# Performance work log

Hardware: AMD Instinct MI355X
Metric: run time of the kernel (lower is better)

The kernel has to match this reference:

```python
import jax, jax.numpy as jnp
import numpy as np

N_ORDER = 256
PRED_LEN = 192
SEQ_LEN = 768
ENC_IN = 21
BATCH = 16
MULTISCALE = [1, 2, 4]
MODES = 32  # min(32, min(pred_len, seq_len)//2)


def _transition(N):
    Q = np.arange(N, dtype=np.float64)
    R = (2 * Q + 1)[:, None]
    j, i = np.meshgrid(Q, Q)
    A = np.where(i < j, -1, (-1.0) ** (i - j + 1)) * R
    B = (-1.0) ** Q[:, None] * R
    return A, B


def _bilinear(A, B, dt):
    # scipy cont2discrete(method='bilinear'): Ad=(I-dt/2 A)^-1 (I+dt/2 A), Bd=(I-dt/2 A)^-1 dt B
    N = A.shape[0]
    I = np.eye(N)
    ima = I - (dt / 2.0) * A
    Ad = np.linalg.solve(ima, I + (dt / 2.0) * A)
    Bd = np.linalg.solve(ima, dt * B)
    return Ad, Bd.squeeze(-1)


def _legendre_eval(N, x):
    # Legendre P_n(x) via three-term recurrence; returns [len(x), N]
    T = x.shape[0]
    P = np.zeros((N, T))
    P[0] = 1.0
    if N > 1:
        P[1] = x
    for n in range(2, N):
        P[n] = ((2 * n - 1) * x * P[n - 1] - (n - 1) * P[n - 2]) / n
    return P.T


def setup_inputs() -> dict:
    key = jax.random.key(0)
    ks = jax.random.split(key, 12)
    inp = {"x_enc": jax.random.normal(ks[0], (BATCH, SEQ_LEN, ENC_IN), dtype=jnp.float32)}
    Ac, Bc = _transition(N_ORDER)
    scale = 1.0 / (N_ORDER * N_ORDER)
    for idx, m in enumerate(MULTISCALE):
        dt = 1.0 / PRED_LEN / m
        Ad, Bd = _bilinear(Ac, Bc, dt)
        vals = np.arange(0.0, 1.0, dt)
        E = _legendre_eval(N_ORDER, 1.0 - 2.0 * vals)
        inp[f"A{idx}"] = jnp.asarray(Ad, jnp.float32)
        inp[f"B{idx}"] = jnp.asarray(Bd, jnp.float32)
        inp[f"E{idx}"] = jnp.asarray(E, jnp.float32)
        inp[f"Wr{idx}"] = scale * jax.random.uniform(ks[1 + 2 * idx], (N_ORDER, N_ORDER, MODES), dtype=jnp.float32)
        inp[f"Wi{idx}"] = scale * jax.random.uniform(ks[2 + 2 * idx], (N_ORDER, N_ORDER, MODES), dtype=jnp.float32)
    inp["mlp_w"] = 0.1 * jax.random.normal(ks[10], (1, len(MULTISCALE)), dtype=jnp.float32)
    inp["mlp_b"] = jnp.zeros((1,), jnp.float32)
    return inp


def _hippo(x, A, Bv):
    # x: [B, E, L]; c_t = c_{t-1} @ A^T + f_t * B  (F.linear(c, A) == c @ A.T)
    def step(c, f):
        c = c @ A.T + f[..., None] * Bv
        return c, c
    c0 = jnp.zeros(x.shape[:-1] + (A.shape[0],), x.dtype)
    _, cs = jax.lax.scan(step, c0, jnp.moveaxis(x, -1, 0))
    return jnp.moveaxis(cs, 0, -1)  # [B, E, N, L]


def _spec_conv(x, Wr, Wi):
    # x: [B, E, N_in, L]; keep first MODES rfft modes, complex channel mix, irfft
    L = x.shape[-1]
    a = jnp.fft.rfft(x, axis=-1)[..., :MODES]
    W = (Wr + 1j * Wi).astype(jnp.complex64)
    out = jnp.einsum('bjix,iox->bjox', a, W)
    nf = L // 2 + 1
    out_full = jnp.pad(out, ((0, 0), (0, 0), (0, 0), (0, nf - MODES)))
    return jnp.fft.irfft(out_full, n=L, axis=-1)


def reference(x_enc, A0, B0, E0, Wr0, Wi0, A1, B1, E1, Wr1, Wi1, A2, B2, E2, Wr2, Wi2, mlp_w, mlp_b):
    params = [(A0, B0, E0, Wr0, Wi0), (A1, B1, E1, Wr1, Wi1), (A2, B2, E2, Wr2, Wi2)]
    x_decs = []
    for m, (A, Bv, E, Wr, Wi) in zip(MULTISCALE, params):
        x_in = x_enc[:, -m * PRED_LEN:]                      # [B, L, E]
        c = _hippo(jnp.transpose(x_in, (0, 2, 1)), A, Bv)    # [B, E, N, L]
        out1 = _spec_conv(c, Wr, Wi)                         # [B, E, N, L]
        x_dec_c = out1[:, :, :, PRED_LEN - 1]                # seq_len >= pred_len, jump_dist=0
        x_decs.append(x_dec_c @ E[-PRED_LEN:].T)             # [B, E, pred_len]
    x_dec = jnp.stack(x_decs, axis=-1)                       # [B, E, pred_len, 3]
    out = x_dec @ mlp_w[0] + mlp_b[0]                        # Linear(3,1) then squeeze
    return jnp.transpose(out, (0, 2, 1))                     # [B, pred_len, E]
```

## Files before the change

### kernel.cpp

```cpp
#include <hip/hip_runtime.h>
#include <math.h>

#define PI_F 3.14159265358979323846f

#define W_OFF    0
#define AP_OFF   344064
#define KT_OFF   737280
#define KTOT_OFF 995328
#define Y_OFF    1142784
#define S_OFF    1142784
#define F_OFF    1732608
#define QT_OFF   10579968
#define WS_FLOATS 27095040

__device__ __forceinline__ int off_w_f(int s)  { return 49152  * ((1 << s) - 1); }
__device__ __forceinline__ int qoff_f(int s)   { return 2359296 * ((1 << s) - 1); }
__device__ __forceinline__ int ktoff_f(int s)  { return 36864  * ((1 << s) - 1); }
__device__ __forceinline__ int foff_f(int s)   { return 1179648 * ((1 << s) - 1); }

template<bool BT>
__device__ __forceinline__ void gemm_tile(const float* __restrict__ A,
                                          const float* __restrict__ B,
                                          float* __restrict__ C,
                                          int M, int N, int ldc, int m0, int n0)
{
    __shared__ float As[16][68];
    __shared__ float Bs[16][68];
    const int tid = threadIdx.x;
    const int tx = tid & 15;
    const int ty = tid >> 4;
    const int r  = tid >> 2;
    const int kq = (tid & 3) << 2;

    float acc[4][4] = {{0.f,0.f,0.f,0.f},{0.f,0.f,0.f,0.f},
                       {0.f,0.f,0.f,0.f},{0.f,0.f,0.f,0.f}};

    for (int kk = 0; kk < 256; kk += 16) {
        float4 av = make_float4(0.f, 0.f, 0.f, 0.f);
        if (m0 + r < M)
            av = *(const float4*)(A + (size_t)(m0 + r) * 256 + kk + kq);
        As[kq + 0][r] = av.x; As[kq + 1][r] = av.y;
        As[kq + 2][r] = av.z; As[kq + 3][r] = av.w;

        if (BT) {
            float4 bv = make_float4(0.f, 0.f, 0.f, 0.f);
            if (n0 + r < N)
                bv = *(const float4*)(B + (size_t)(n0 + r) * 256 + kk + kq);
            Bs[kq + 0][r] = bv.x; Bs[kq + 1][r] = bv.y;
            Bs[kq + 2][r] = bv.z; Bs[kq + 3][r] = bv.w;
        } else {
            const int kb = tid >> 4;
            const int j4 = (tid & 15) << 2;
            float4 bv = *(const float4*)(B + (size_t)(kk + kb) * 256 + n0 + j4);
            *(float4*)(&Bs[kb][j4]) = bv;
        }
        __syncthreads();

        #pragma unroll
        for (int k = 0; k < 16; ++k) {
            float4 a4 = *(const float4*)(&As[k][ty << 2]);
            float4 b4 = *(const float4*)(&Bs[k][tx << 2]);
            acc[0][0] = fmaf(a4.x, b4.x, acc[0][0]);
            acc[0][1] = fmaf(a4.x, b4.y, acc[0][1]);
            acc[0][2] = fmaf(a4.x, b4.z, acc[0][2]);
            acc[0][3] = fmaf(a4.x, b4.w, acc[0][3]);
            acc[1][0] = fmaf(a4.y, b4.x, acc[1][0]);
            acc[1][1] = fmaf(a4.y, b4.y, acc[1][1]);
            acc[1][2] = fmaf(a4.y, b4.z, acc[1][2]);
            acc[1][3] = fmaf(a4.y, b4.w, acc[1][3]);
            acc[2][0] = fmaf(a4.z, b4.x, acc[2][0]);
            acc[2][1] = fmaf(a4.z, b4.y, acc[2][1]);
            acc[2][2] = fmaf(a4.z, b4.z, acc[2][2]);
            acc[2][3] = fmaf(a4.z, b4.w, acc[2][3]);
            acc[3][0] = fmaf(a4.w, b4.x, acc[3][0]);
            acc[3][1] = fmaf(a4.w, b4.y, acc[3][1]);
            acc[3][2] = fmaf(a4.w, b4.z, acc[3][2]);
            acc[3][3] = fmaf(a4.w, b4.w, acc[3][3]);
        }
        __syncthreads();
    }

    #pragma unroll
    for (int u = 0; u < 4; ++u) {
        int row = m0 + (ty << 2) + u;
        if (row < M) {
            float4 cv = make_float4(acc[u][0], acc[u][1], acc[u][2], acc[u][3]);
            *(float4*)(C + (size_t)row * ldc + n0 + (tx << 2)) = cv;
        }
    }
}

__device__ __forceinline__ void gemm_64x256(const float* __restrict__ A,
                                            const float* __restrict__ B,
                                            float* __restrict__ C, int ldc)
{
    __shared__ float As[16][68];
    __shared__ float Bs[16][260];

    const int tid = threadIdx.x;
    const int tx = tid & 15;
    const int ty = tid >> 4;
    const int ra  = tid >> 2;
    const int kqa = (tid & 3) << 2;

    float acc[4][4][4];
    #pragma unroll
    for (int j = 0; j < 4; ++j)
        #pragma unroll
        for (int u = 0; u < 4; ++u)
            #pragma unroll
            for (int v = 0; v < 4; ++v) acc[j][u][v] = 0.f;

    for (int kk = 0; kk < 256; kk += 16) {
        float4 av = *(const float4*)(A + (size_t)ra * 256 + kk + kqa);
        As[kqa + 0][ra] = av.x; As[kqa + 1][ra] = av.y;
        As[kqa + 2][ra] = av.z; As[kqa + 3][ra] = av.w;

        const float* bp = B + (size_t)tid * 256 + kk;
        float4 b0 = *(const float4*)(bp);
        float4 b1 = *(const float4*)(bp + 4);
        float4 b2 = *(const float4*)(bp + 8);
        float4 b3 = *(const float4*)(bp + 12);
        Bs[ 0][tid] = b0.x; Bs[ 1][tid] = b0.y; Bs[ 2][tid] = b0.z; Bs[ 3][tid] = b0.w;
        Bs[ 4][tid] = b1.x; Bs[ 5][tid] = b1.y; Bs[ 6][tid] = b1.z; Bs[ 7][tid] = b1.w;
        Bs[ 8][tid] = b2.x; Bs[ 9][tid] = b2.y; Bs[10][tid] = b2.z; Bs[11][tid] = b2.w;
        Bs[12][tid] = b3.x; Bs[13][tid] = b3.y; Bs[14][tid] = b3.z; Bs[15][tid] = b3.w;
        __syncthreads();

        #pragma unroll
        for (int kq = 0; kq < 16; ++kq) {
            float4 a  = *(const float4*)(&As[kq][4 * ty]);
            float4 c0 = *(const float4*)(&Bs[kq][4 * tx]);
            float4 c1 = *(const float4*)(&Bs[kq][4 * tx + 64]);
            float4 c2 = *(const float4*)(&Bs[kq][4 * tx + 128]);
            float4 c3 = *(const float4*)(&Bs[kq][4 * tx + 192]);
            float af[4]  = {a.x, a.y, a.z, a.w};
            float bf[16] = {c0.x, c0.y, c0.z, c0.w, c1.x, c1.y, c1.z, c1.w,
                            c2.x, c2.y, c2.z, c2.w, c3.x, c3.y, c3.z, c3.w};
            #pragma unroll
            for (int j = 0; j < 4; ++j)
                #pragma unroll
                for (int u = 0; u < 4; ++u)
                    #pragma unroll
                    for (int v = 0; v < 4; ++v)
                        acc[j][u][v] = fmaf(af[u], bf[j * 4 + v], acc[j][u][v]);
        }
        __syncthreads();
    }

    #pragma unroll
    for (int u = 0; u < 4; ++u) {
        int row = 4 * ty + u;
        #pragma unroll
        for (int j = 0; j < 4; ++j) {
            float4 cv = make_float4(acc[j][u][0], acc[j][u][1],
                                    acc[j][u][2], acc[j][u][3]);
            *(float4*)(C + (size_t)row * ldc + 4 * tx + 64 * j) = cv;
        }
    }
}

__global__ void k_init(const float* B0, const float* B1, const float* B2, float* ws)
{
    int s = blockIdx.x;
    const float* Bv = (s == 0) ? B0 : (s == 1) ? B1 : B2;
    ws[W_OFF + off_w_f(s) + threadIdx.x] = Bv[threadIdx.x];
}

__global__ void k_level(int n, const float* A0, const float* A1, const float* A2,
                        float* ws)
{
    int s = blockIdx.z;
    int L = 192 << s;
    const float* Ain = (s == 0) ? A0 : (s == 1) ? A1 : A2;
    float* wbase = ws + W_OFF + off_w_f(s);
    float* bufA  = ws + AP_OFF + s * 131072;
    float* bufB  = bufA + 65536;
    const float* src = (n == 0) ? Ain : (((n - 1) & 1) ? bufB : bufA);

    int y = blockIdx.y;
    if (y < 4) {
        int p2 = 1 << n;
        if (p2 >= L) return;
        int cnt = min(p2, L - p2);
        int m0 = y * 64;
        if (m0 >= cnt) return;
        gemm_tile<true>(wbase, src, wbase + (size_t)p2 * 256,
                        cnt, 256, 256, m0, blockIdx.x * 64);
    } else {
        if ((2 << n) >= L) return;
        float* dst = (n & 1) ? bufB : bufA;
        gemm_tile<false>(src, src, dst, 256, 256, 256, (y - 4) * 64, blockIdx.x * 64);
    }
}

__global__ void k_transpose(const float* Wr0, const float* Wi0,
                            const float* Wr1, const float* Wi1,
                            const float* Wr2, const float* Wi2, float* ws)
{
    int bid = blockIdx.x;
    int i  = bid & 255;
    int ri = (bid >> 8) & 1;
    int s  = bid >> 9;
    const float* W;
    if (s == 0)      W = ri ? Wi0 : Wr0;
    else if (s == 1) W = ri ? Wi1 : Wr1;
    else             W = ri ? Wi2 : Wr2;

    int o = threadIdx.x;
    int sri = s * 2 + ri;
    const float* Wrow = W + (size_t)i * 8192 + (size_t)o * 32;
    #pragma unroll
    for (int k = 0; k < 32; ++k) {
        ws[QT_OFF + ((size_t)(sri * 32 + k) * 256 + i) * 256 + o] = Wrow[k];
    }
}

__global__ void __launch_bounds__(256, 2)
k_gemm_Y3(const float* E0, const float* E1, const float* E2, float* __restrict__ ws)
{
    const int zz = blockIdx.x;
    const int s  = blockIdx.z;
    const int L  = 192 << s;
    const int z  = s * 64 + zz;
    const int m0 = blockIdx.y * 64;
    const float* E = (s == 0) ? E0 : (s == 1) ? E1 : E2;

    const float* Ap = E + (size_t)(L - 192) * 256 + (size_t)m0 * 256;
    const float* Bp = ws + QT_OFF + (size_t)z * 65536;
    float* Cp = ws + Y_OFF + (size_t)z * 49152 + (size_t)m0 * 256;
    gemm_64x256(Ap, Bp, Cp, 256);
}

__global__ void __launch_bounds__(256, 2)
k_gemm_Q3(float* __restrict__ ws)
{
    const int s = blockIdx.z;
    const int L = 192 << s;
    const int m0 = blockIdx.y * 64;
    if (m0 >= L) return;
    const int n0 = blockIdx.x * 256;

    const float* Ap = ws + W_OFF + off_w_f(s) + (size_t)m0 * 256;
    const float* Bp = ws + Y_OFF + (size_t)s * 3145728 + (size_t)n0 * 256;
    float* Cp = ws + QT_OFF + qoff_f(s) + (size_t)m0 * 12288 + n0;
    gemm_64x256(Ap, Bp, Cp, 12288);
}

__global__ void k_scanA(float* __restrict__ ws)
{
    const int c = blockIdx.x;
    const int k = blockIdx.y;
    const int s = blockIdx.z;
    const int L = 192 << s;
    const int C = L >> 4;
    const int p = threadIdx.x;

    __shared__ float twc[768], tws[768];
    for (int m = p; m < L; m += 192) {
        float ang = -2.f * PI_F * (float)m / (float)L;
        float ss, cc; sincosf(ang, &ss, &cc);
        twc[m] = cc; tws[m] = ss;
    }
    __syncthreads();

    const float* Qr = ws + QT_OFF + qoff_f(s) + (size_t)k * 192;
    const float* Qi = Qr + 6144;

    float ar = 0.f, ai = 0.f;
    const int d0 = c * C;
    int ph = (k * d0) % L;
    for (int j = 0; j < C; ++j) {
        int d = d0 + j;
        float qr = Qr[(size_t)d * 12288 + p];
        float qi = Qi[(size_t)d * 12288 + p];
        float cc = twc[ph], sn = tws[ph];
        ar = fmaf(cc, qr, fmaf(-sn, qi, ar));
        ai = fmaf(cc, qi, fmaf( sn, qr, ai));
        ph += k; if (ph >= L) ph -= L;
    }
    size_t sb = (size_t)((s * 32 + k) * 16 + c) * 384;
    ws[S_OFF + sb + p]       = ar;
    ws[S_OFF + sb + 192 + p] = ai;
}

__global__ void k_scanB(float* __restrict__ ws)
{
    const int c = blockIdx.x;
    const int k = blockIdx.y;
    const int s = blockIdx.z;
    const int L = 192 << s;
    const int C = L >> 4;
    const int p = threadIdx.x;

    __shared__ float twc[768], tws[768];
    for (int m = p; m < L; m += 192) {
        float ang = -2.f * PI_F * (float)m / (float)L;
        float ss, cc; sincosf(ang, &ss, &cc);
        twc[m] = cc; tws[m] = ss;
    }
    __syncthreads();

    float ar = 0.f, ai = 0.f;
    size_t sbase = (size_t)(s * 32 + k) * 16 * 384;
    for (int c2 = 0; c2 < c; ++c2) {
        ar += ws[S_OFF + sbase + (size_t)c2 * 384 + p];
        ai += ws[S_OFF + sbase + (size_t)c2 * 384 + 192 + p];
    }

    const float ck = ((k == 0) ? 1.f : 2.f) / (float)L;
    const float* Qr = ws + QT_OFF + qoff_f(s) + (size_t)k * 192;
    const float* Qi = Qr + 6144;
    float* F = ws + F_OFF + foff_f(s);

    const int d0 = c * C;
    int ph = (k * d0) % L;
    int m1 = d0 + 192 - L; if (m1 < 0) m1 += L;
    int ph2 = (k * m1) % L;
    for (int j = 0; j < C; ++j) {
        int d = d0 + j;
        float qr = Qr[(size_t)d * 12288 + p];
        float qi = Qi[(size_t)d * 12288 + p];
        float cc = twc[ph], sn = tws[ph];
        ar = fmaf(cc, qr, fmaf(-sn, qi, ar));
        ai = fmaf(cc, qi, fmaf( sn, qr, ai));
        float f = ck * fmaf(twc[ph2], ar, tws[ph2] * ai);
        int sidx = L - 1 - d;
        F[((size_t)sidx * 32 + k) * 192 + p] = f;
        ph  += k; if (ph  >= L) ph  -= L;
        ph2 += k; if (ph2 >= L) ph2 -= L;
    }
}

__global__ void k_kred(float* __restrict__ ws)
{
    int bid = blockIdx.x;
    int s, sidx;
    if (bid < 192)      { s = 0; sidx = bid; }
    else if (bid < 576) { s = 1; sidx = bid - 192; }
    else                { s = 2; sidx = bid - 576; }
    int p = threadIdx.x;
    const float* F = ws + F_OFF + foff_f(s) + (size_t)sidx * 32 * 192;
    float sum = 0.f;
    #pragma unroll
    for (int k = 0; k < 32; ++k)
        sum += F[k * 192 + p];
    ws[KT_OFF + ktoff_f(s) + (size_t)sidx * 192 + p] = sum;
}

__global__ void k_combine(float* ws, const float* mw)
{
    int idx = blockIdx.x * 256 + threadIdx.x;
    if (idx >= 147456) return;
    int tau = idx / 192;
    int p   = idx - tau * 192;
    float sum = 0.f;
    #pragma unroll
    for (int s = 0; s < 3; ++s) {
        int L = 192 << s;
        int off = 768 - L;
        if (tau >= off)
            sum = fmaf(mw[s], ws[KT_OFF + ktoff_f(s) + (size_t)(tau - off) * 192 + p], sum);
    }
    ws[KTOT_OFF + idx] = sum;
}

__global__ void k_out(const float* __restrict__ x, const float* __restrict__ ws,
                      const float* __restrict__ mb, float* __restrict__ out)
{
    int bid = blockIdx.x;
    int b = bid / 21;
    int c = bid - b * 21;
    __shared__ float xl[768];
    for (int t = threadIdx.x; t < 768; t += 192)
        xl[t] = x[((size_t)b * 768 + t) * 21 + c];
    __syncthreads();

    int p = threadIdx.x;
    const float* K = ws + KTOT_OFF;
    float acc = 0.f;
    for (int tau = 0; tau < 768; ++tau)
        acc = fmaf(xl[tau], K[(size_t)tau * 192 + p], acc);
    out[((size_t)b * 192 + p) * 21 + c] = acc + mb[0];
}

extern "C" void kernel_launch(void* const* d_in, const int* in_sizes, int n_in,
                              void* d_out, int out_size, void* d_ws, size_t ws_size,
                              hipStream_t stream)
{
    const float* x   = (const float*)d_in[0];
    const float* A0  = (const float*)d_in[1];
    const float* B0  = (const float*)d_in[2];
    const float* E0  = (const float*)d_in[3];
    const float* Wr0 = (const float*)d_in[4];
    const float* Wi0 = (const float*)d_in[5];
    const float* A1  = (const float*)d_in[6];
    const float* B1  = (const float*)d_in[7];
    const float* E1  = (const float*)d_in[8];
    const float* Wr1 = (const float*)d_in[9];
    const float* Wi1 = (const float*)d_in[10];
    const float* A2  = (const float*)d_in[11];
    const float* B2  = (const float*)d_in[12];
    const float* E2  = (const float*)d_in[13];
    const float* Wr2 = (const float*)d_in[14];
    const float* Wi2 = (const float*)d_in[15];
    const float* mw  = (const float*)d_in[16];
    const float* mb  = (const float*)d_in[17];
    float* ws  = (float*)d_ws;
    float* out = (float*)d_out;

    if (ws_size < (size_t)WS_FLOATS * sizeof(float)) {
        hipMemsetAsync(d_out, 0, (size_t)out_size * sizeof(float), stream);
        return;
    }

    k_init<<<3, 256, 0, stream>>>(B0, B1, B2, ws);
    for (int n = 0; n < 10; ++n)
        k_level<<<dim3(4, 8, 3), 256, 0, stream>>>(n, A0, A1, A2, ws);
    k_transpose<<<1536, 256, 0, stream>>>(Wr0, Wi0, Wr1, Wi1, Wr2, Wi2, ws);
    k_gemm_Y3<<<dim3(64, 3, 3), 256, 0, stream>>>(E0, E1, E2, ws);
    k_gemm_Q3<<<dim3(48, 12, 3), 256, 0, stream>>>(ws);
    k_scanA<<<dim3(16, 32, 3), 192, 0, stream>>>(ws);
    k_scanB<<<dim3(16, 32, 3), 192, 0, stream>>>(ws);
    k_kred<<<1344, 192, 0, stream>>>(ws);
    k_combine<<<576, 256, 0, stream>>>(ws, mw);
    k_out<<<336, 192, 0, stream>>>(x, ws, mb, out);
}
```

Measured before the change: 488.5 us.

## Fuse k-mode reduction into scan via atomics and compact GEMM grids

The scan kernel now accumulates its per-mode outputs straight into the Kt buffer with atomicAdd, so the large F intermediate and the separate k_kred reduction kernel go away. A zeroing kernel is added to clear Kt first. The two GEMM launches are reshaped into 1D/2D grids with no idle blocks, and their launch bounds are raised to 4 blocks per SM. The change cuts F buffer traffic and one launch, but brings 32-way atomic contention per element and a nondeterministic summation order.

```diff
diff --git a/kernel.cpp b/kernel.cpp
--- a/kernel.cpp
+++ b/kernel.cpp
@@ -9,14 +9,12 @@
 #define KTOT_OFF 995328
 #define Y_OFF    1142784
 #define S_OFF    1142784
-#define F_OFF    1732608
 #define QT_OFF   10579968
 #define WS_FLOATS 27095040
 
 __device__ __forceinline__ int off_w_f(int s)  { return 49152  * ((1 << s) - 1); }
 __device__ __forceinline__ int qoff_f(int s)   { return 2359296 * ((1 << s) - 1); }
 __device__ __forceinline__ int ktoff_f(int s)  { return 36864  * ((1 << s) - 1); }
-__device__ __forceinline__ int foff_f(int s)   { return 1179648 * ((1 << s) - 1); }
 
 template<bool BT>
 __device__ __forceinline__ void gemm_tile(const float* __restrict__ A,
@@ -167,6 +165,13 @@
     ws[W_OFF + off_w_f(s) + threadIdx.x] = Bv[threadIdx.x];
 }
 
+__global__ void k_zero_ktil(float* ws)
+{
+    int idx = blockIdx.x * 256 + threadIdx.x;
+    float4 z = make_float4(0.f, 0.f, 0.f, 0.f);
+    *(float4*)(ws + KT_OFF + (size_t)idx * 4) = z;
+}
+
 __global__ void k_level(int n, const float* A0, const float* A1, const float* A2,
                         float* ws)
 {
@@ -216,13 +221,12 @@
     }
 }
 
-__global__ void __launch_bounds__(256, 2)
-k_gemm_Y3(const float* E0, const float* E1, const float* E2, float* __restrict__ ws)
-{
-    const int zz = blockIdx.x;
-    const int s  = blockIdx.z;
+__global__ void __launch_bounds__(256, 4)
+k_gemm_Y5(const float* E0, const float* E1, const float* E2, float* __restrict__ ws)
+{
+    const int z  = blockIdx.x;
+    const int s  = z >> 6;
     const int L  = 192 << s;
-    const int z  = s * 64 + zz;
     const int m0 = blockIdx.y * 64;
     const float* E = (s == 0) ? E0 : (s == 1) ? E1 : E2;
 
@@ -232,13 +236,15 @@
     gemm_64x256(Ap, Bp, Cp, 256);
 }
 
-__global__ void __launch_bounds__(256, 2)
-k_gemm_Q3(float* __restrict__ ws)
-{
-    const int s = blockIdx.z;
-    const int L = 192 << s;
-    const int m0 = blockIdx.y * 64;
-    if (m0 >= L) return;
+__global__ void __launch_bounds__(256, 4)
+k_gemm_Q5(float* __restrict__ ws)
+{
+    const int y = blockIdx.y;
+    int s, yt;
+    if (y < 3)      { s = 0; yt = y; }
+    else if (y < 9) { s = 1; yt = y - 3; }
+    else            { s = 2; yt = y - 9; }
+    const int m0 = yt * 64;
     const int n0 = blockIdx.x * 256;
 
     const float* Ap = ws + W_OFF + off_w_f(s) + (size_t)m0 * 256;
@@ -311,7 +317,7 @@
     const float ck = ((k == 0) ? 1.f : 2.f) / (float)L;
     const float* Qr = ws + QT_OFF + qoff_f(s) + (size_t)k * 192;
     const float* Qi = Qr + 6144;
-    float* F = ws + F_OFF + foff_f(s);
+    float* Kt = ws + KT_OFF + ktoff_f(s);
 
     const int d0 = c * C;
     int ph = (k * d0) % L;
@@ -326,26 +332,10 @@
         ai = fmaf(cc, qi, fmaf( sn, qr, ai));
         float f = ck * fmaf(twc[ph2], ar, tws[ph2] * ai);
         int sidx = L - 1 - d;
-        F[((size_t)sidx * 32 + k) * 192 + p] = f;
+        atomicAdd(Kt + (size_t)sidx * 192 + p, f);
         ph  += k; if (ph  >= L) ph  -= L;
         ph2 += k; if (ph2 >= L) ph2 -= L;
     }
-}
-
-__global__ void k_kred(float* __restrict__ ws)
-{
-    int bid = blockIdx.x;
-    int s, sidx;
-    if (bid < 192)      { s = 0; sidx = bid; }
-    else if (bid < 576) { s = 1; sidx = bid - 192; }
-    else                { s = 2; sidx = bid - 576; }
-    int p = threadIdx.x;
-    const float* F = ws + F_OFF + foff_f(s) + (size_t)sidx * 32 * 192;
-    float sum = 0.f;
-    #pragma unroll
-    for (int k = 0; k < 32; ++k)
-        sum += F[k * 192 + p];
-    ws[KT_OFF + ktoff_f(s) + (size_t)sidx * 192 + p] = sum;
 }
 
 __global__ void k_combine(float* ws, const float* mw)
@@ -415,14 +405,14 @@
     }
 
     k_init<<<3, 256, 0, stream>>>(B0, B1, B2, ws);
+    k_zero_ktil<<<252, 256, 0, stream>>>(ws);
     for (int n = 0; n < 10; ++n)
         k_level<<<dim3(4, 8, 3), 256, 0, stream>>>(n, A0, A1, A2, ws);
     k_transpose<<<1536, 256, 0, stream>>>(Wr0, Wi0, Wr1, Wi1, Wr2, Wi2, ws);
-    k_gemm_Y3<<<dim3(64, 3, 3), 256, 0, stream>>>(E0, E1, E2, ws);
-    k_gemm_Q3<<<dim3(48, 12, 3), 256, 0, stream>>>(ws);
+    k_gemm_Y5<<<dim3(192, 3), 256, 0, stream>>>(E0, E1, E2, ws);
+    k_gemm_Q5<<<dim3(48, 21), 256, 0, stream>>>(ws);
     k_scanA<<<dim3(16, 32, 3), 192, 0, stream>>>(ws);
     k_scanB<<<dim3(16, 32, 3), 192, 0, stream>>>(ws);
-    k_kred<<<1344, 192, 0, stream>>>(ws);
     k_combine<<<576, 256, 0, stream>>>(ws, mw);
     k_out<<<336, 192, 0, stream>>>(x, ws, mb, out);
 }
```

After: 501.1 us. +2.6%, slower.
